# Optimization experiments

Measured on AMD Instinct MI355X. Metric: run time of the kernel, lower is better.

The kernel has to match this reference:

```python
import jax, jax.numpy as jnp
import numpy as np

S, B, E, H, V = 512, 256, 256, 256, 50000


def setup_inputs() -> dict:
    key = jax.random.key(0)
    ks = jax.random.split(key, 16)
    sc = 0.05
    return {
        "s1": jax.random.randint(ks[0], (S, B), 0, V, dtype=jnp.int32),
        "s2": jax.random.randint(ks[1], (S, B), 0, V, dtype=jnp.int32),
        "emb": jax.random.normal(ks[2], (V, E), jnp.float32) * sc,
        "W_ih": jax.random.normal(ks[3], (4 * H, E), jnp.float32) * sc,
        "W_hh": jax.random.normal(ks[4], (4 * H, H), jnp.float32) * sc,
        "b_ih": jax.random.normal(ks[5], (4 * H,), jnp.float32) * sc,
        "b_hh": jax.random.normal(ks[6], (4 * H,), jnp.float32) * sc,
        "h0_1": jax.random.normal(ks[7], (B, H), jnp.float32),
        "c0_1": jax.random.normal(ks[8], (B, H), jnp.float32),
        "h0_2": jax.random.normal(ks[9], (B, H), jnp.float32),
        "c0_2": jax.random.normal(ks[10], (B, H), jnp.float32),
        "W1": jax.random.normal(ks[11], (H, 2 * H), jnp.float32) * sc,
        "b1": jax.random.normal(ks[12], (H,), jnp.float32) * sc,
        "W2": jax.random.normal(ks[13], (2, H), jnp.float32) * sc,
        "b2": jax.random.normal(ks[14], (2,), jnp.float32) * sc,
    }


def _lstm(tokens, emb, W_ih, W_hh, b_ih, b_hh, h0, c0):
    # tokens: [S, B] int; returns final hidden h: [B, H]
    x = emb[tokens]  # [S, B, E]
    b = b_ih + b_hh

    def step(carry, xt):
        h, c = carry
        gates = xt @ W_ih.T + h @ W_hh.T + b  # [B, 4H]
        i, f, g, o = jnp.split(gates, 4, axis=-1)  # PyTorch gate order
        i = jax.nn.sigmoid(i)
        f = jax.nn.sigmoid(f)
        g = jnp.tanh(g)
        o = jax.nn.sigmoid(o)
        c = f * c + i * g
        h = o * jnp.tanh(c)
        return (h, c), None

    (h, c), _ = jax.lax.scan(step, (h0, c0), x)
    return h


def reference(s1, s2, emb, W_ih, W_hh, b_ih, b_hh, h0_1, c0_1, h0_2, c0_2, W1, b1, W2, b2):
    v1 = _lstm(s1, emb, W_ih, W_hh, b_ih, b_hh, h0_1, c0_1)  # [B, H]
    v2 = _lstm(s2, emb, W_ih, W_hh, b_ih, b_hh, h0_2, c0_2)  # [B, H]
    feat = jnp.concatenate([v1, v2], axis=-1)  # [B, 2H]
    hid = feat @ W1.T + b1  # no activation, per original Sequential
    out = hid @ W2.T + b2  # [B, 2]
    return out
```

## Files before the change

kernel.cpp:

```cpp
#include <hip/hip_runtime.h>
#include <hip/hip_bf16.h>

#define SS 512
#define BB 256
#define EE 256
#define HH 256
#define VV 50000
#define NCH 512
#define NB 4
#define NWG (NCH / NB)
#define VR 16

__device__ __forceinline__ float sigf(float x) { return 1.f / (1.f + __expf(-x)); }
__device__ __forceinline__ float tanhf_fast(float x) { return 1.f - 2.f / (__expf(2.f * x) + 1.f); }

__global__ void pack_w4(const float* __restrict__ W, float4* __restrict__ Wp, int K) {
    int idx = blockIdx.x * blockDim.x + threadIdx.x;
    if (idx >= K * HH) return;
    int k = idx >> 8, t = idx & 255;
    Wp[idx] = make_float4(W[(0 * HH + t) * K + k], W[(1 * HH + t) * K + k],
                          W[(2 * HH + t) * K + k], W[(3 * HH + t) * K + k]);
}

__global__ void pack_b(const float* __restrict__ bi, const float* __restrict__ bh,
                       float4* __restrict__ bp) {
    int t = threadIdx.x;
    bp[t] = make_float4(bi[0 * HH + t] + bh[0 * HH + t], bi[1 * HH + t] + bh[1 * HH + t],
                        bi[2 * HH + t] + bh[2 * HH + t], bi[3 * HH + t] + bh[3 * HH + t]);
}

__global__ void transpose_w1(const float* __restrict__ W1, float* __restrict__ W1T) {
    int idx = blockIdx.x * blockDim.x + threadIdx.x;
    if (idx >= 2 * HH * HH) return;
    int k = idx >> 8, j = idx & 255;
    W1T[idx] = W1[j * (2 * HH) + k];
}

__global__ __launch_bounds__(256) void embw_kernel(const float* __restrict__ emb,
                                                   const float4* __restrict__ Wip,
                                                   const float4* __restrict__ bp,
                                                   float4* __restrict__ embWp) {
    __shared__ float se[VR][EE];
    int t = threadIdx.x;
    int v0 = blockIdx.x * VR;
    for (int r = 0; r < VR; ++r) se[r][t] = emb[(size_t)(v0 + r) * EE + t];
    __syncthreads();
    float4 bb = bp[t];
    float4 acc[VR];
#pragma unroll
    for (int r = 0; r < VR; ++r) acc[r] = bb;
#pragma unroll 2
    for (int k = 0; k < EE; ++k) {
        float4 w = Wip[k * HH + t];
#pragma unroll
        for (int r = 0; r < VR; ++r) {
            float x = se[r][k];
            acc[r].x += w.x * x; acc[r].y += w.y * x;
            acc[r].z += w.z * x; acc[r].w += w.w * x;
        }
    }
    for (int r = 0; r < VR; ++r) embWp[(size_t)(v0 + r) * HH + t] = acc[r];
}

template <bool PRE>
__global__ __launch_bounds__(256, 1) void lstm_kernel(
    const int* __restrict__ s1, const int* __restrict__ s2, const float* __restrict__ emb,
    const float4* __restrict__ Whp, const float4* __restrict__ Wip,
    const float4* __restrict__ bp, const float4* __restrict__ embWp,
    const float* __restrict__ h0_1, const float* __restrict__ c0_1,
    const float* __restrict__ h0_2, const float* __restrict__ c0_2,
    float* __restrict__ feat) {
    __shared__ float hs[NB][HH];
    __shared__ int tok_lds[SS * NB];
    int t = threadIdx.x;
    int ch0 = blockIdx.x * NB;

    float c[NB];
    int bat[NB];
    const int* toks[NB];
#pragma unroll
    for (int nb = 0; nb < NB; ++nb) {
        int ch = ch0 + nb;
        bool t2 = ch >= BB;
        int b = t2 ? ch - BB : ch;
        bat[nb] = b;
        toks[nb] = t2 ? s2 : s1;
        const float* h0 = t2 ? h0_2 : h0_1;
        const float* cc0 = t2 ? c0_2 : c0_1;
        hs[nb][t] = h0[b * HH + t];
        c[nb] = cc0[b * HH + t];
    }
    for (int idx = t; idx < SS * NB; idx += 256) {
        int s = idx >> 2, nb = idx & 3;
        tok_lds[idx] = toks[nb][s * BB + bat[nb]];
    }
    __syncthreads();

    float4 pf[NB];
    if constexpr (PRE) {
#pragma unroll
        for (int nb = 0; nb < NB; ++nb)
            pf[nb] = embWp[(size_t)tok_lds[nb] * HH + t];
    }

    for (int s = 0; s < SS; ++s) {
        float4 acc[NB];
        if constexpr (PRE) {
#pragma unroll
            for (int nb = 0; nb < NB; ++nb) acc[nb] = pf[nb];
            if (s + 1 < SS) {
#pragma unroll
                for (int nb = 0; nb < NB; ++nb)
                    pf[nb] = embWp[(size_t)tok_lds[(s + 1) * NB + nb] * HH + t];
            }
        } else {
            __shared__ float xs[NB][EE];
            float4 bb = bp[t];
#pragma unroll
            for (int nb = 0; nb < NB; ++nb) {
                int tok = tok_lds[s * NB + nb];
                xs[nb][t] = emb[(size_t)tok * EE + t];
                acc[nb] = bb;
            }
            __syncthreads();
#pragma unroll 4
            for (int k = 0; k < EE; ++k) {
                float4 w = Wip[k * HH + t];
#pragma unroll
                for (int nb = 0; nb < NB; ++nb) {
                    float x = xs[nb][k];
                    acc[nb].x += w.x * x; acc[nb].y += w.y * x;
                    acc[nb].z += w.z * x; acc[nb].w += w.w * x;
                }
            }
        }
#pragma unroll 8
        for (int k = 0; k < HH; ++k) {
            float4 w = Whp[k * HH + t];
#pragma unroll
            for (int nb = 0; nb < NB; ++nb) {
                float hk = hs[nb][k];
                acc[nb].x += w.x * hk; acc[nb].y += w.y * hk;
                acc[nb].z += w.z * hk; acc[nb].w += w.w * hk;
            }
        }
        float hnew[NB];
#pragma unroll
        for (int nb = 0; nb < NB; ++nb) {
            float ig = sigf(acc[nb].x);
            float fg = sigf(acc[nb].y);
            float gg = tanhf_fast(acc[nb].z);
            float og = sigf(acc[nb].w);
            c[nb] = fg * c[nb] + ig * gg;
            hnew[nb] = og * tanhf_fast(c[nb]);
        }
        __syncthreads();
#pragma unroll
        for (int nb = 0; nb < NB; ++nb) hs[nb][t] = hnew[nb];
        __syncthreads();
    }
#pragma unroll
    for (int nb = 0; nb < NB; ++nb) feat[(size_t)(ch0 + nb) * HH + t] = hs[nb][t];
}

__global__ __launch_bounds__(256) void head_kernel(const float* __restrict__ feat,
                                                   const float* __restrict__ W1T,
                                                   const float* __restrict__ b1,
                                                   const float* __restrict__ W2,
                                                   const float* __restrict__ b2,
                                                   float* __restrict__ out) {
    __shared__ float f[2 * HH];
    __shared__ float r0[256], r1[256];
    int j = threadIdx.x;
    int b = blockIdx.x;
    f[j] = feat[(size_t)b * HH + j];
    f[HH + j] = feat[(size_t)(BB + b) * HH + j];
    __syncthreads();
    float acc = b1[j];
#pragma unroll 4
    for (int k = 0; k < 2 * HH; ++k) acc += f[k] * W1T[k * HH + j];
    r0[j] = acc * W2[0 * HH + j];
    r1[j] = acc * W2[1 * HH + j];
    __syncthreads();
    for (int st = 128; st > 0; st >>= 1) {
        if (j < st) { r0[j] += r0[j + st]; r1[j] += r1[j + st]; }
        __syncthreads();
    }
    if (j == 0) {
        out[b * 2 + 0] = r0[0] + b2[0];
        out[b * 2 + 1] = r1[0] + b2[1];
    }
}

extern "C" void kernel_launch(void* const* d_in, const int* in_sizes, int n_in,
                              void* d_out, int out_size, void* d_ws, size_t ws_size,
                              hipStream_t stream) {
    const int* s1 = (const int*)d_in[0];
    const int* s2 = (const int*)d_in[1];
    const float* emb = (const float*)d_in[2];
    const float* W_ih = (const float*)d_in[3];
    const float* W_hh = (const float*)d_in[4];
    const float* b_ih = (const float*)d_in[5];
    const float* b_hh = (const float*)d_in[6];
    const float* h0_1 = (const float*)d_in[7];
    const float* c0_1 = (const float*)d_in[8];
    const float* h0_2 = (const float*)d_in[9];
    const float* c0_2 = (const float*)d_in[10];
    const float* W1 = (const float*)d_in[11];
    const float* b1 = (const float*)d_in[12];
    const float* W2 = (const float*)d_in[13];
    const float* b2 = (const float*)d_in[14];
    float* out = (float*)d_out;

    char* ws = (char*)d_ws;
    size_t off = 0;
    auto alloc = [&](size_t bytes) {
        void* p = ws + off;
        off += (bytes + 255) & ~(size_t)255;
        return p;
    };
    float4* Whp = (float4*)alloc((size_t)HH * HH * sizeof(float4));
    float4* Wip = (float4*)alloc((size_t)EE * HH * sizeof(float4));
    float4* bp = (float4*)alloc(HH * sizeof(float4));
    float* W1T = (float*)alloc((size_t)2 * HH * HH * sizeof(float));
    float* feat = (float*)alloc((size_t)NCH * HH * sizeof(float));
    size_t embw_bytes = (size_t)VV * HH * sizeof(float4);
    bool pre = (ws_size >= off + embw_bytes);
    float4* embWp = pre ? (float4*)alloc(embw_bytes) : nullptr;

    pack_w4<<<(HH * HH + 255) / 256, 256, 0, stream>>>(W_ih, Wip, EE);
    pack_w4<<<(HH * HH + 255) / 256, 256, 0, stream>>>(W_hh, Whp, HH);
    pack_b<<<1, 256, 0, stream>>>(b_ih, b_hh, bp);
    transpose_w1<<<(2 * HH * HH + 255) / 256, 256, 0, stream>>>(W1, W1T);

    if (pre) {
        embw_kernel<<<VV / VR, 256, 0, stream>>>(emb, Wip, bp, embWp);
        lstm_kernel<true><<<NWG, 256, 0, stream>>>(s1, s2, emb, Whp, Wip, bp, embWp,
                                                   h0_1, c0_1, h0_2, c0_2, feat);
    } else {
        lstm_kernel<false><<<NWG, 256, 0, stream>>>(s1, s2, emb, Whp, Wip, bp, embWp,
                                                    h0_1, c0_1, h0_2, c0_2, feat);
    }
    head_kernel<<<BB, 256, 0, stream>>>(feat, W1T, b1, W2, b2, out);
}
```

Measured before the change: 5.772 ms.

## Split LSTM hidden dimension across cooperating workgroups with global-memory step barriers

Replaces the per-workgroup LSTM, where each of 128 blocks streams the full W_hh from global memory every step for 4 sequences, with 256 workgroups arranged as 32 groups by 8 hidden-dimension slices. Each workgroup keeps its 32-column slice of W_hh resident in LDS (128 KB) and exchanges h through a double-buffered global array, with an atomic counter barrier per group each timestep. The aim is to use more CUs and cut repeated global or L2 weight traffic. In exchange it adds a cross-workgroup spin barrier every step, which needs all 256 blocks co-resident and has a timeout fallback that could silently give wrong results.

```diff
diff --git a/kernel.cpp b/kernel.cpp
--- a/kernel.cpp
+++ b/kernel.cpp
@@ -7,9 +7,10 @@
 #define HH 256
 #define VV 50000
 #define NCH 512
-#define NB 4
-#define NWG (NCH / NB)
 #define VR 16
+
+#define NGRP 32
+#define NSLC 8
 
 __device__ __forceinline__ float sigf(float x) { return 1.f / (1.f + __expf(-x)); }
 __device__ __forceinline__ float tanhf_fast(float x) { return 1.f - 2.f / (__expf(2.f * x) + 1.f); }
@@ -34,6 +35,11 @@
     if (idx >= 2 * HH * HH) return;
     int k = idx >> 8, j = idx & 255;
     W1T[idx] = W1[j * (2 * HH) + k];
+}
+
+__global__ void zero_cnt(int* __restrict__ cnt) {
+    int t = threadIdx.x;
+    if (t < NGRP) cnt[t] = 0;
 }
 
 __global__ __launch_bounds__(256) void embw_kernel(const float* __restrict__ emb,
@@ -62,105 +68,217 @@
     for (int r = 0; r < VR; ++r) embWp[(size_t)(v0 + r) * HH + t] = acc[r];
 }
 
-template <bool PRE>
-__global__ __launch_bounds__(256, 1) void lstm_kernel(
+__global__ __launch_bounds__(256, 1) void lstm_coop(
+    const int* __restrict__ s1, const int* __restrict__ s2,
+    const float4* __restrict__ Whp, const float4* __restrict__ embWp,
+    const float* __restrict__ h0_1, const float* __restrict__ c0_1,
+    const float* __restrict__ h0_2, const float* __restrict__ c0_2,
+    float* __restrict__ feat, float* __restrict__ hbuf, int* __restrict__ cnt) {
+    __shared__ float4 w4s[256 * 32];
+    __shared__ float4 hls4[256 * 4];
+
+    const int bid = blockIdx.x;
+    const int g = bid & (NGRP - 1);
+    const int u = bid >> 5;
+    const int t = threadIdx.x;
+    const int j = t & 31, ks = (t >> 5) & 1, mg = t >> 6;
+    const int u32j = u * 32 + j;
+
+    for (int idx = t; idx < 256 * 32; idx += 256)
+        w4s[idx] = Whp[(idx >> 5) * HH + u * 32 + (idx & 31)];
+
+    const bool tw2 = g >= 16;
+    const float* h0x = tw2 ? h0_2 : h0_1;
+    const float* c0x = tw2 ? c0_2 : c0_1;
+    const int* tp = tw2 ? s2 : s1;
+    const int gb = (g & 15) * 16;
+
+    float* hptr = (float*)hls4;
+#pragma unroll
+    for (int q = 0; q < 16; ++q) {
+        int e = t + q * 256;
+        hptr[e] = h0x[(gb + (e & 15)) * HH + (e >> 4)];
+    }
+    float c[4];
+#pragma unroll
+    for (int i = 0; i < 4; ++i) c[i] = c0x[(gb + mg * 4 + i) * HH + u32j];
+    __syncthreads();
+
+    const int bq0 = gb + mg * 4 + 2 * ks;
+    float4 pfv[2]; int tnx[2];
+    {
+        int tk0 = tp[0 * BB + bq0], tk1 = tp[0 * BB + bq0 + 1];
+        pfv[0] = embWp[(size_t)tk0 * HH + u32j];
+        pfv[1] = embWp[(size_t)tk1 * HH + u32j];
+        tnx[0] = tp[1 * BB + bq0];
+        tnx[1] = tp[1 * BB + bq0 + 1];
+    }
+
+    const float4* wp = w4s + ks * 128 * 32 + j;
+    const float4* hp = hls4 + ks * 128 * 4 + mg;
+    const int chg0 = g * 16 + mg * 4;
+    int dead = 0;
+
+    for (int s = 0; s < SS; ++s) {
+        float4 pf2[2]; int t2[2];
+        pf2[0] = embWp[(size_t)tnx[0] * HH + u32j];
+        pf2[1] = embWp[(size_t)tnx[1] * HH + u32j];
+        int sn = (s + 2 < SS) ? s + 2 : SS - 1;
+        t2[0] = tp[sn * BB + bq0];
+        t2[1] = tp[sn * BB + bq0 + 1];
+
+        float4 a0 = {0, 0, 0, 0}, a1 = {0, 0, 0, 0}, a2 = {0, 0, 0, 0}, a3 = {0, 0, 0, 0};
+#pragma unroll 4
+        for (int kk = 0; kk < 128; ++kk) {
+            float4 w = wp[kk * 32];
+            float4 h4 = hp[kk * 4];
+            a0.x += w.x * h4.x; a0.y += w.y * h4.x; a0.z += w.z * h4.x; a0.w += w.w * h4.x;
+            a1.x += w.x * h4.y; a1.y += w.y * h4.y; a1.z += w.z * h4.y; a1.w += w.w * h4.y;
+            a2.x += w.x * h4.z; a2.y += w.y * h4.z; a2.z += w.z * h4.z; a2.w += w.w * h4.z;
+            a3.x += w.x * h4.w; a3.y += w.y * h4.w; a3.z += w.z * h4.w; a3.w += w.w * h4.w;
+        }
+        if (ks == 0) {
+            a0.x += pfv[0].x; a0.y += pfv[0].y; a0.z += pfv[0].z; a0.w += pfv[0].w;
+            a1.x += pfv[1].x; a1.y += pfv[1].y; a1.z += pfv[1].z; a1.w += pfv[1].w;
+        } else {
+            a2.x += pfv[0].x; a2.y += pfv[0].y; a2.z += pfv[0].z; a2.w += pfv[0].w;
+            a3.x += pfv[1].x; a3.y += pfv[1].y; a3.z += pfv[1].z; a3.w += pfv[1].w;
+        }
+        a0.x += __shfl_xor(a0.x, 32); a0.y += __shfl_xor(a0.y, 32);
+        a0.z += __shfl_xor(a0.z, 32); a0.w += __shfl_xor(a0.w, 32);
+        a1.x += __shfl_xor(a1.x, 32); a1.y += __shfl_xor(a1.y, 32);
+        a1.z += __shfl_xor(a1.z, 32); a1.w += __shfl_xor(a1.w, 32);
+        a2.x += __shfl_xor(a2.x, 32); a2.y += __shfl_xor(a2.y, 32);
+        a2.z += __shfl_xor(a2.z, 32); a2.w += __shfl_xor(a2.w, 32);
+        a3.x += __shfl_xor(a3.x, 32); a3.y += __shfl_xor(a3.y, 32);
+        a3.z += __shfl_xor(a3.z, 32); a3.w += __shfl_xor(a3.w, 32);
+
+        float hn[4];
+        {
+            float ig, fg, gg, og;
+            ig = sigf(a0.x); fg = sigf(a0.y); gg = tanhf_fast(a0.z); og = sigf(a0.w);
+            c[0] = fg * c[0] + ig * gg; hn[0] = og * tanhf_fast(c[0]);
+            ig = sigf(a1.x); fg = sigf(a1.y); gg = tanhf_fast(a1.z); og = sigf(a1.w);
+            c[1] = fg * c[1] + ig * gg; hn[1] = og * tanhf_fast(c[1]);
+            ig = sigf(a2.x); fg = sigf(a2.y); gg = tanhf_fast(a2.z); og = sigf(a2.w);
+            c[2] = fg * c[2] + ig * gg; hn[2] = og * tanhf_fast(c[2]);
+            ig = sigf(a3.x); fg = sigf(a3.y); gg = tanhf_fast(a3.z); og = sigf(a3.w);
+            c[3] = fg * c[3] + ig * gg; hn[3] = og * tanhf_fast(c[3]);
+        }
+        float* hdst = hbuf + ((s + 1) & 1) * (NCH * HH);
+        if (ks == 0) {
+            hdst[(chg0 + 0) * HH + u32j] = hn[0];
+            hdst[(chg0 + 1) * HH + u32j] = hn[1];
+            hdst[(chg0 + 2) * HH + u32j] = hn[2];
+            hdst[(chg0 + 3) * HH + u32j] = hn[3];
+        }
+        __threadfence();
+        __syncthreads();
+        if (t == 0) {
+            atomicAdd(&cnt[g], 1);
+            int tgt = NSLC * (s + 1);
+            if (!dead) {
+                long it = 0;
+                while (__hip_atomic_load(&cnt[g], __ATOMIC_RELAXED,
+                                         __HIP_MEMORY_SCOPE_AGENT) < tgt) {
+                    if (++it >= 4000000L) { dead = 1; break; }
+                    __builtin_amdgcn_s_sleep(2);
+                }
+            }
+        }
+        __syncthreads();
+        __threadfence();
+        const float* hsrc = hbuf + ((s + 1) & 1) * (NCH * HH) + (g * 16) * HH;
+#pragma unroll
+        for (int q = 0; q < 16; ++q) {
+            int e = t + q * 256;
+            hptr[e] = hsrc[(e & 15) * HH + (e >> 4)];
+        }
+        __syncthreads();
+        pfv[0] = pf2[0]; pfv[1] = pf2[1];
+        tnx[0] = t2[0]; tnx[1] = t2[1];
+    }
+
+    if (u == 0) {
+#pragma unroll
+        for (int q = 0; q < 16; ++q) {
+            int e = t + q * 256;
+            feat[(size_t)(g * 16 + (e & 15)) * HH + (e >> 4)] = hptr[e];
+        }
+    }
+}
+
+#define NBF 4
+__global__ __launch_bounds__(256, 1) void lstm_stream(
     const int* __restrict__ s1, const int* __restrict__ s2, const float* __restrict__ emb,
     const float4* __restrict__ Whp, const float4* __restrict__ Wip,
-    const float4* __restrict__ bp, const float4* __restrict__ embWp,
+    const float4* __restrict__ bp,
     const float* __restrict__ h0_1, const float* __restrict__ c0_1,
     const float* __restrict__ h0_2, const float* __restrict__ c0_2,
     float* __restrict__ feat) {
-    __shared__ float hs[NB][HH];
-    __shared__ int tok_lds[SS * NB];
+    __shared__ float hs[NBF][HH];
+    __shared__ float xs[NBF][EE];
     int t = threadIdx.x;
-    int ch0 = blockIdx.x * NB;
-
-    float c[NB];
-    int bat[NB];
-    const int* toks[NB];
-#pragma unroll
-    for (int nb = 0; nb < NB; ++nb) {
+    int ch0 = blockIdx.x * NBF;
+    float c[NBF];
+    int bat[NBF];
+    const int* toks[NBF];
+#pragma unroll
+    for (int nb = 0; nb < NBF; ++nb) {
         int ch = ch0 + nb;
         bool t2 = ch >= BB;
         int b = t2 ? ch - BB : ch;
         bat[nb] = b;
         toks[nb] = t2 ? s2 : s1;
-        const float* h0 = t2 ? h0_2 : h0_1;
-        const float* cc0 = t2 ? c0_2 : c0_1;
-        hs[nb][t] = h0[b * HH + t];
-        c[nb] = cc0[b * HH + t];
-    }
-    for (int idx = t; idx < SS * NB; idx += 256) {
-        int s = idx >> 2, nb = idx & 3;
-        tok_lds[idx] = toks[nb][s * BB + bat[nb]];
-    }
-    __syncthreads();
-
-    float4 pf[NB];
-    if constexpr (PRE) {
-#pragma unroll
-        for (int nb = 0; nb < NB; ++nb)
-            pf[nb] = embWp[(size_t)tok_lds[nb] * HH + t];
-    }
-
+        hs[nb][t] = (t2 ? h0_2 : h0_1)[b * HH + t];
+        c[nb] = (t2 ? c0_2 : c0_1)[b * HH + t];
+    }
+    __syncthreads();
     for (int s = 0; s < SS; ++s) {
-        float4 acc[NB];
-        if constexpr (PRE) {
-#pragma unroll
-            for (int nb = 0; nb < NB; ++nb) acc[nb] = pf[nb];
-            if (s + 1 < SS) {
-#pragma unroll
-                for (int nb = 0; nb < NB; ++nb)
-                    pf[nb] = embWp[(size_t)tok_lds[(s + 1) * NB + nb] * HH + t];
-            }
-        } else {
-            __shared__ float xs[NB][EE];
-            float4 bb = bp[t];
-#pragma unroll
-            for (int nb = 0; nb < NB; ++nb) {
-                int tok = tok_lds[s * NB + nb];
-                xs[nb][t] = emb[(size_t)tok * EE + t];
-                acc[nb] = bb;
-            }
-            __syncthreads();
+        float4 acc[NBF];
+        float4 bb = bp[t];
+#pragma unroll
+        for (int nb = 0; nb < NBF; ++nb) {
+            int tok = toks[nb][s * BB + bat[nb]];
+            xs[nb][t] = emb[(size_t)tok * EE + t];
+            acc[nb] = bb;
+        }
+        __syncthreads();
 #pragma unroll 4
-            for (int k = 0; k < EE; ++k) {
-                float4 w = Wip[k * HH + t];
-#pragma unroll
-                for (int nb = 0; nb < NB; ++nb) {
-                    float x = xs[nb][k];
-                    acc[nb].x += w.x * x; acc[nb].y += w.y * x;
-                    acc[nb].z += w.z * x; acc[nb].w += w.w * x;
-                }
+        for (int k = 0; k < EE; ++k) {
+            float4 w = Wip[k * HH + t];
+#pragma unroll
+            for (int nb = 0; nb < NBF; ++nb) {
+                float x = xs[nb][k];
+                acc[nb].x += w.x * x; acc[nb].y += w.y * x;
+                acc[nb].z += w.z * x; acc[nb].w += w.w * x;
             }
         }
 #pragma unroll 8
         for (int k = 0; k < HH; ++k) {
             float4 w = Whp[k * HH + t];
 #pragma unroll
-            for (int nb = 0; nb < NB; ++nb) {
+            for (int nb = 0; nb < NBF; ++nb) {
                 float hk = hs[nb][k];
                 acc[nb].x += w.x * hk; acc[nb].y += w.y * hk;
                 acc[nb].z += w.z * hk; acc[nb].w += w.w * hk;
             }
         }
-        float hnew[NB];
-#pragma unroll
-        for (int nb = 0; nb < NB; ++nb) {
-            float ig = sigf(acc[nb].x);
-            float fg = sigf(acc[nb].y);
-            float gg = tanhf_fast(acc[nb].z);
-            float og = sigf(acc[nb].w);
+        float hnew[NBF];
+#pragma unroll
+        for (int nb = 0; nb < NBF; ++nb) {
+            float ig = sigf(acc[nb].x), fg = sigf(acc[nb].y);
+            float gg = tanhf_fast(acc[nb].z), og = sigf(acc[nb].w);
             c[nb] = fg * c[nb] + ig * gg;
             hnew[nb] = og * tanhf_fast(c[nb]);
         }
         __syncthreads();
 #pragma unroll
-        for (int nb = 0; nb < NB; ++nb) hs[nb][t] = hnew[nb];
-        __syncthreads();
-    }
-#pragma unroll
-    for (int nb = 0; nb < NB; ++nb) feat[(size_t)(ch0 + nb) * HH + t] = hs[nb][t];
+        for (int nb = 0; nb < NBF; ++nb) hs[nb][t] = hnew[nb];
+        __syncthreads();
+    }
+#pragma unroll
+    for (int nb = 0; nb < NBF; ++nb) feat[(size_t)(ch0 + nb) * HH + t] = hs[nb][t];
 }
 
 __global__ __launch_bounds__(256) void head_kernel(const float* __restrict__ feat,
@@ -224,6 +342,8 @@
     float4* bp = (float4*)alloc(HH * sizeof(float4));
     float* W1T = (float*)alloc((size_t)2 * HH * HH * sizeof(float));
     float* feat = (float*)alloc((size_t)NCH * HH * sizeof(float));
+    float* hbuf = (float*)alloc((size_t)2 * NCH * HH * sizeof(float));
+    int* cnt = (int*)alloc(NGRP * sizeof(int));
     size_t embw_bytes = (size_t)VV * HH * sizeof(float4);
     bool pre = (ws_size >= off + embw_bytes);
     float4* embWp = pre ? (float4*)alloc(embw_bytes) : nullptr;
@@ -234,12 +354,14 @@
     transpose_w1<<<(2 * HH * HH + 255) / 256, 256, 0, stream>>>(W1, W1T);
 
     if (pre) {
+        zero_cnt<<<1, 128, 0, stream>>>(cnt);
         embw_kernel<<<VV / VR, 256, 0, stream>>>(emb, Wip, bp, embWp);
-        lstm_kernel<true><<<NWG, 256, 0, stream>>>(s1, s2, emb, Whp, Wip, bp, embWp,
+        lstm_coop<<<NGRP * NSLC, 256, 0, stream>>>(s1, s2, Whp, embWp,
+                                                   h0_1, c0_1, h0_2, c0_2,
+                                                   feat, hbuf, cnt);
+    } else {
+        lstm_stream<<<NCH / NBF, 256, 0, stream>>>(s1, s2, emb, Whp, Wip, bp,
                                                    h0_1, c0_1, h0_2, c0_2, feat);
-    } else {
-        lstm_kernel<false><<<NWG, 256, 0, stream>>>(s1, s2, emb, Whp, Wip, bp, embWp,
-                                                    h0_1, c0_1, h0_2, c0_2, feat);
     }
     head_kernel<<<BB, 256, 0, stream>>>(feat, W1T, b1, W2, b2, out);
 }
```

After: 22.78 ms. +294.6%, slower.
